# Performance work log

Measured on AMD Instinct MI355X. Metric: run time of the kernel, lower is better.

## Reference

```python
import jax, jax.numpy as jnp
from jax import lax
import numpy as np

# Config mirroring init_kwargs
B, N, PD = 4, 16384, 3
PROJ = 64                 # projection_channel
M1, K1, C1 = 2048, 32, 128  # level-1 SA: fps points, neighbors, out channel
M2, K2, C2 = 512, 32, 256   # level-2 SA
DH, DO = 512, 256           # dense hidden / out (dense_channels)


def fps(pts, M):
    """Farthest point sampling. pts: [N,3] -> indices [M] (starts at point 0)."""
    n = pts.shape[0]
    def step(carry, _):
        dmin, last = carry
        d = jnp.sum((pts - pts[last]) ** 2, axis=-1)   # dist to newest center
        dmin = jnp.minimum(dmin, d)
        nxt = jnp.argmax(dmin).astype(jnp.int32)
        return (dmin, nxt), last
    init = (jnp.full((n,), 1e10, pts.dtype), jnp.int32(0))
    _, idxs = lax.scan(step, init, None, length=M)
    return idxs


def sa_level(pts, feats, M, K, Wa, ba, Wb, bb):
    """PointNet++ set abstraction: FPS + kNN (xyz space) + grouped MLP + max."""
    idx = jax.vmap(lambda p: fps(p, M))(pts)                       # [B,M]
    centers = jnp.take_along_axis(pts, idx[:, :, None], axis=1)    # [B,M,3]
    d = jnp.sum((centers[:, :, None, :] - pts[:, None, :, :]) ** 2, -1)  # [B,M,N]
    _, nidx = lax.top_k(-d, K)                                      # [B,M,K]
    gather = jax.vmap(lambda a, i: a[i])
    rel = gather(pts, nidx) - centers[:, :, None, :]                # [B,M,K,3]
    nf = gather(feats, nidx)                                        # [B,M,K,C]
    g = jnp.concatenate([rel, nf], axis=-1)                         # use_xyz=True
    h = jax.nn.relu(g @ Wa + ba)
    h = jax.nn.relu(h @ Wb + bb)
    return centers, jnp.max(h, axis=2)                              # [B,M,Cout]


def setup_inputs() -> dict:
    key = jax.random.key(0)
    ks = jax.random.split(key, 12)
    w = lambda k, shape, s: jax.random.normal(k, shape, jnp.float32) * s
    z = lambda c: jnp.zeros((c,), jnp.float32)
    return {
        "xyz": jax.random.normal(ks[0], (B, N, PD), jnp.float32),
        "Wp": w(ks[1], (PD, PROJ), 0.3), "bp": z(PROJ),
        "W1a": w(ks[2], (PROJ + 3, C1), 0.1), "b1a": z(C1),
        "W1b": w(ks[3], (C1, C1), 0.08), "b1b": z(C1),
        "W2a": w(ks[4], (C1 + 3, C2), 0.08), "b2a": z(C2),
        "W2b": w(ks[5], (C2, C2), 0.06), "b2b": z(C2),
        "Wd1": w(ks[6], (2 * C2, DH), 0.05), "bd1": z(DH),
        "Wd2": w(ks[7], (DH, DO), 0.05), "bd2": z(DO),
    }


def reference(xyz, Wp, bp, W1a, b1a, W1b, b1b, W2a, b2a, W2b, b2b,
              Wd1, bd1, Wd2, bd2):
    feats = xyz @ Wp + bp            # point_proj: [B,N,PROJ]
    pts = xyz[..., :3]
    pts, feats = sa_level(pts, feats, M1, K1, W1a, b1a, W1b, b1b)
    pts, feats = sa_level(pts, feats, M2, K2, W2a, b2a, W2b, b2b)
    # global max + avg pool (adaptive_max/avg_pool1d to 1), concat -> [B,2*C2]
    g = jnp.concatenate([jnp.max(feats, axis=1), jnp.mean(feats, axis=1)], -1)
    h = jax.nn.relu(g @ Wd1 + bd1)   # DenseBlock w/ activation
    return h @ Wd2 + bd2             # last block: no activation (last_activation=False)
```

## Files before the change

### kernel.cpp

```cpp
#include <hip/hip_runtime.h>

#define B_    4
#define N1_   16384
#define M1_   2048
#define M2_   512
#define KNN_  32
#define PROJ_ 64
#define C1_   128
#define C2_   256
#define PROJ_BLKS_ ((B_ * N1_ * PROJ_) / 512)
#define TAIL_BLKS_ (32 * 512)

__device__ __forceinline__ float sqdist_exact(float px, float py, float pz,
                                              float cx, float cy, float cz) {
    float dx = __fsub_rn(px, cx);
    float dy = __fsub_rn(py, cy);
    float dz = __fsub_rn(pz, cz);
    return __fadd_rn(__fadd_rn(__fmul_rn(dx, dx), __fmul_rn(dy, dy)), __fmul_rn(dz, dz));
}

__device__ __forceinline__ float aload(const float* p) {
    return __uint_as_float(__hip_atomic_load((const unsigned*)p,
                           __ATOMIC_RELAXED, __HIP_MEMORY_SCOPE_AGENT));
}
__device__ __forceinline__ unsigned auload(const unsigned* p) {
    return __hip_atomic_load(p, __ATOMIC_RELAXED, __HIP_MEMORY_SCOPE_AGENT);
}
__device__ __forceinline__ void afence() {
    __builtin_amdgcn_fence(__ATOMIC_ACQUIRE, "agent");
}

#define F_PROG1(f,b)  ((f) + (b) * 16)
#define F_PROG2(f,b)  ((f) + 64 + (b) * 16)
#define F_PROJD(f)    ((f) + 128)
#define F_K1D(f,b,c)  ((f) + 192 + ((b) * 32 + (c)) * 16)
#define F_M2D(f,b)    ((f) + 2240 + (b) * 16)
#define F_K2D(f,b,c)  ((f) + 2304 + ((b) * 8 + (c)) * 16)

__global__ void __launch_bounds__(1024)
sortx_kernel(const float* __restrict__ xyz, float* __restrict__ sx,
             float* __restrict__ sy, float* __restrict__ sz,
             float* __restrict__ sp) {
    const int b = blockIdx.x, t = threadIdx.x;
    const int lane = t & 63, w = t >> 6;
    const float* P = xyz + (size_t)b * N1_ * 3;
    __shared__ int hist[1024];
    __shared__ int wsum[16];
    hist[t] = 0;
    __syncthreads();
    for (int j = t; j < N1_; j += 1024) {
        unsigned kb = __float_as_uint(P[j * 3]);
        kb ^= (kb >> 31) ? 0xFFFFFFFFu : 0x80000000u;
        atomicAdd(&hist[kb >> 22], 1);
    }
    __syncthreads();
    int v = hist[t];
    int cum = v;
    for (int off = 1; off < 64; off <<= 1) {
        int o = __shfl_up(cum, off);
        if (lane >= off) cum += o;
    }
    if (lane == 63) wsum[w] = cum;
    __syncthreads();
    int wpre = 0;
    for (int i = 0; i < w; ++i) wpre += wsum[i];
    const int excl = cum - v + wpre;
    __syncthreads();
    hist[t] = excl;
    __syncthreads();
    for (int j = t; j < N1_; j += 1024) {
        float x = P[j * 3], y = P[j * 3 + 1], z = P[j * 3 + 2];
        unsigned kb = __float_as_uint(x);
        kb ^= (kb >> 31) ? 0xFFFFFFFFu : 0x80000000u;
        int pos = atomicAdd(&hist[kb >> 22], 1);
        size_t o = (size_t)b * N1_ + pos;
        sx[o] = x; sy[o] = y; sz[o] = z;
        float* pr = sp + ((size_t)b * N1_ + pos) * 3;
        pr[0] = x; pr[1] = y; pr[2] = z;
    }
}

typedef float v2f __attribute__((ext_vector_type(2)));

template<int CTRL, int RM>
__device__ __forceinline__ unsigned long long dpp_umax64(unsigned long long pk) {
    unsigned lo = (unsigned)__builtin_amdgcn_update_dpp(
        0, (int)(unsigned)pk, CTRL, RM, 0xf, true);
    unsigned hi = (unsigned)__builtin_amdgcn_update_dpp(
        0, (int)(unsigned)(pk >> 32), CTRL, RM, 0xf, true);
    unsigned long long o = ((unsigned long long)hi << 32) | (unsigned long long)lo;
    return (o > pk) ? o : pk;
}

__device__ __forceinline__ unsigned long long wave_max_key(unsigned long long pk) {
    pk = dpp_umax64<0x111, 0xf>(pk);
    pk = dpp_umax64<0x112, 0xf>(pk);
    pk = dpp_umax64<0x114, 0xf>(pk);
    pk = dpp_umax64<0x118, 0xf>(pk);
    pk = dpp_umax64<0x142, 0xa>(pk);
    pk = dpp_umax64<0x143, 0xc>(pk);
    return pk;
}

__device__ __forceinline__ unsigned reduce8_widx(const unsigned long long* wk,
                                                 int lane) {
    unsigned long long k8 = wk[lane & 7];
    k8 = dpp_umax64<0x111, 0xf>(k8);
    k8 = dpp_umax64<0x112, 0xf>(k8);
    k8 = dpp_umax64<0x114, 0xf>(k8);
    unsigned lo = (unsigned)__builtin_amdgcn_readlane((int)(unsigned)k8, 7);
    return ~lo;
}

__device__ __forceinline__ unsigned reduce4_widx(const unsigned long long* wk,
                                                 int lane) {
    unsigned long long k4 = wk[lane & 3];
    k4 = dpp_umax64<0x111, 0xf>(k4);
    k4 = dpp_umax64<0x112, 0xf>(k4);
    unsigned lo = (unsigned)__builtin_amdgcn_readlane((int)(unsigned)k4, 3);
    return ~lo;
}

template<int N, int NT>
__device__ void knn_bodyT(const float* __restrict__ P,
                          float cx, float cy, float cz,
                          int* __restrict__ out, char* arena) {
    constexpr int K = KNN_;
    constexpr int CAP = 224;
    const int t = threadIdx.x;
    const int lane = t & 63;
    const int w = t >> 6;

    int*      hist = (int*)arena;
    unsigned* eqk  = (unsigned*)(arena + 8192);
    int*      eqi  = (int*)(arena + 8192 + 896);
    int*      wsum = (int*)(arena + 8192 + 1792);
    int*      ctrl = (int*)(arena + 8192 + 1824);

    unsigned prefix = 0; int pbits = 0;
    unsigned Tlo = 0; unsigned long long Thi = 0x100000000ull;
    int L = 0, target = K, Cbin = N;

    for (int round = 0; round < 3; ++round) {
        const int bits  = (round < 2) ? 11 : 10;
        const int nbins = 1 << bits;
        const int shift = 32 - pbits - bits;
        for (int i = t; i < nbins; i += NT) hist[i] = 0;
        __syncthreads();
        for (int j = t; j < N; j += NT) {
            float d = sqdist_exact(P[j * 3], P[j * 3 + 1], P[j * 3 + 2], cx, cy, cz);
            unsigned key = __float_as_uint(d);
            if (key >= Tlo && (unsigned long long)key < Thi)
                atomicAdd(&hist[(key >> shift) & (nbins - 1)], 1);
        }
        __syncthreads();
        const int per = nbins / NT;
        int s = 0;
        for (int i = 0; i < per; ++i) s += hist[t * per + i];
        int cum = s;
        for (int off = 1; off < 64; off <<= 1) {
            int o = __shfl_up(cum, off);
            if (lane >= off) cum += o;
        }
        if (lane == 63) wsum[w] = cum;
        __syncthreads();
        int wpre = 0;
        for (int i = 0; i < w; ++i) wpre += wsum[i];
        cum += wpre;
        const int cumex = cum - s;
        if ((cumex < target) && (cum >= target)) {
            int acc = cumex;
            for (int i = 0; i < per; ++i) {
// ... 108 lines not shown
        const float w2 = Wa[(4 * s4 + 5) * CO + o];
        const float w3 = Wa[(4 * s4 + 6) * CO + o];
#pragma unroll
        for (int k = 0; k < 8; ++k) {
            float4 gv = *(const float4*)&g[k0 + k][4 * s4];
            acc[k] = __fmaf_rn(gv.x, w0, acc[k]);
            acc[k] = __fmaf_rn(gv.y, w1, acc[k]);
            acc[k] = __fmaf_rn(gv.z, w2, acc[k]);
            acc[k] = __fmaf_rn(gv.w, w3, acc[k]);
        }
    }
    {
        const float w0 = Wa[0 * CO + o];
        const float w1 = Wa[1 * CO + o];
        const float w2 = Wa[2 * CO + o];
#pragma unroll
        for (int k = 0; k < 8; ++k) {
            float4 gv = *(const float4*)&g[k0 + k][FD];
            acc[k] = __fmaf_rn(gv.x, w0, acc[k]);
            acc[k] = __fmaf_rn(gv.y, w1, acc[k]);
            acc[k] = __fmaf_rn(gv.z, w2, acc[k]);
        }
    }
#pragma unroll
    for (int k = 0; k < 8; ++k) h1[k0 + k][o] = fmaxf(acc[k], 0.f);
    __syncthreads();
#pragma unroll
    for (int k = 0; k < 8; ++k) acc[k] = bb[o];
    for (int s4 = 0; s4 < CO / 4; ++s4) {
        const float w0 = Wb[(4 * s4 + 0) * CO + o];
        const float w1 = Wb[(4 * s4 + 1) * CO + o];
        const float w2 = Wb[(4 * s4 + 2) * CO + o];
        const float w3 = Wb[(4 * s4 + 3) * CO + o];
#pragma unroll
        for (int k = 0; k < 8; ++k) {
            float4 hv = *(const float4*)&h1[k0 + k][4 * s4];
            acc[k] = __fmaf_rn(hv.x, w0, acc[k]);
            acc[k] = __fmaf_rn(hv.y, w1, acc[k]);
            acc[k] = __fmaf_rn(hv.z, w2, acc[k]);
            acc[k] = __fmaf_rn(hv.w, w3, acc[k]);
        }
    }
    float mx = 0.f;
#pragma unroll
    for (int k = 0; k < 8; ++k) mx = fmaxf(mx, fmaxf(acc[k], 0.f));
    pm[grp][o] = mx;
    __syncthreads();
    if (t < CO) {
        float m0 = fmaxf(fmaxf(pm[0][o], pm[1][o]), fmaxf(pm[2][o], pm[3][o]));
        feats1[bm * CO + o] = m0;
    }
}

__global__ __attribute__((amdgpu_flat_work_group_size(512, 512)))
__attribute__((amdgpu_waves_per_eu(2, 2)))
void mega1_kernel(const float* __restrict__ xyz,
                  const float* __restrict__ sx, const float* __restrict__ sy,
                  const float* __restrict__ sz, const float* __restrict__ sp,
                  const float* __restrict__ Wp, const float* __restrict__ bp,
                  const float* __restrict__ W1a, const float* __restrict__ b1a,
                  const float* __restrict__ W1b, const float* __restrict__ b1b,
                  float* __restrict__ feats0, float* __restrict__ centers1,
                  int* __restrict__ nidx1, float* __restrict__ feats1,
                  unsigned* __restrict__ flags) {
#pragma clang fp contract(off)
    __shared__ alignas(16) char arena[27136];
    asm volatile("" ::: "v255");
    const int bid = blockIdx.x;
    const int t = threadIdx.x;

    if (bid >= B_ + PROJ_BLKS_) {
        const int k = bid - (B_ + PROJ_BLKS_);
        const int c = k >> 9;
        const int r = k & 511;
        const int i = r & 255;
        const int b = (i >> 6) & 3;
        const int m = c * 64 + (i & 63);
        if (r < 256) {
            if (t == 0) {
                while (auload(F_PROG1(flags, b)) <= (unsigned)c)
                    __builtin_amdgcn_s_sleep(16);
            }
            __syncthreads();
            const float* cw = centers1 + ((size_t)b * M1_ + m) * 3;
            float cx = aload(cw + 0), cy = aload(cw + 1), cz = aload(cw + 2);
            knn_bodyT<N1_, 512>(xyz + (size_t)b * N1_ * 3, cx, cy, cz,
                                nidx1 + ((size_t)b * M1_ + m) * KNN_, arena);
            __syncthreads();
            if (t == 0)
                __hip_atomic_fetch_add(F_K1D(flags, b, c), 1u,
                                       __ATOMIC_RELEASE, __HIP_MEMORY_SCOPE_AGENT);
            return;
        }
        if (t == 0) {
            while (auload(F_K1D(flags, b, c)) < 64u ||
                   auload(F_PROJD(flags)) < (unsigned)PROJ_BLKS_)
                __builtin_amdgcn_s_sleep(16);
        }
        __syncthreads();
        afence();
        mlp1_512(b, m, arena, xyz, feats0, centers1, nidx1,
                 W1a, b1a, W1b, b1b, feats1);
        return;
    }
    if (bid >= B_) {
        int tid = (bid - B_) * 512 + t;
        int cc = tid & (PROJ_ - 1);
        int pn = tid >> 6;
        const float* p = xyz + (size_t)pn * 3;
        float acc = p[0] * Wp[0 * PROJ_ + cc];
        acc = __fmaf_rn(p[1], Wp[1 * PROJ_ + cc], acc);
        acc = __fmaf_rn(p[2], Wp[2 * PROJ_ + cc], acc);
        feats0[tid] = acc + bp[cc];
        __syncthreads();
        if (t == 0)
            __hip_atomic_fetch_add(F_PROJD(flags), 1u,
                                   __ATOMIC_RELEASE, __HIP_MEMORY_SCOPE_AGENT);
        return;
    }
    constexpr int NT = 512;
    constexpr int NW = NT / 64;
    constexpr int PPT = N1_ / NT;
    const int b = bid;
    const int w = t >> 6;
    const int lane = t & 63;
    const float* P  = xyz + (size_t)b * N1_ * 3;
    const float* SX = sx + (size_t)b * N1_;
    const float* SY = sy + (size_t)b * N1_;
    const float* SZ = sz + (size_t)b * N1_;
    const float* SP = sp + (size_t)b * N1_ * 3;
    float* C1 = centers1 + (size_t)b * M1_ * 3;
    const int base = t * PPT;
    const unsigned nbase = ~(unsigned)base;

    unsigned long long (*wkey)[NW] = (unsigned long long(*)[NW])arena;
    float* cb1 = (float*)(arena + 128);

    float px[PPT], py[PPT], pz[PPT], dmin[PPT];
#pragma unroll
    for (int k = 0; k < PPT; ++k) {
        px[k] = SX[base + k];
        py[k] = SY[base + k];
        pz[k] = SZ[base + k];
        dmin[k] = 1e10f;
    }
#pragma unroll
    for (int k = 0; k < PPT; ++k)
        asm volatile("" : "+v"(px[k]), "+v"(py[k]), "+v"(pz[k]), "+v"(dmin[k]));

    float xlo = px[0], xhi = px[0];
#pragma unroll
    for (int k = 1; k < PPT; ++k) {
        xlo = fminf(xlo, px[k]);
        xhi = fmaxf(xhi, px[k]);
    }
    for (int off = 1; off < 64; off <<= 1) {
        xlo = fminf(xlo, __shfl_xor(xlo, off));
        xhi = fmaxf(xhi, __shfl_xor(xhi, off));
    }

    unsigned long long mykey = ((unsigned long long)__float_as_uint(1e10f) << 32);
    float cx = P[0], cy = P[1], cz = P[2];

    for (int m = 0; m < M1_; ++m) {
        if (t == 0) {
            cb1[m * 3 + 0] = cx; cb1[m * 3 + 1] = cy; cb1[m * 3 + 2] = cz;
        }
        if ((m & 63) == 63) {
            __syncthreads();
            const int c = m >> 6;
            if (t < 48)
                ((float4*)C1)[c * 48 + t] = ((const float4*)cb1)[c * 48 + t];
            __syncthreads();
            if (t == 0)
                __hip_atomic_store(F_PROG1(flags, b), (unsigned)(c + 1),
                                   __ATOMIC_RELEASE, __HIP_MEMORY_SCOPE_AGENT);
        }
        if (m == M1_ - 1) break;
        const int par = m & 1;
        const float UBval = __uint_as_float((unsigned)(mykey >> 32));
        const float dxs = fmaxf(fmaxf(xlo - cx, cx - xhi), 0.0f);
        if (!(0.999f * (dxs * dxs) >= UBval)) {
            unsigned long long pk = 0;
#pragma unroll
            for (int k = 0; k < PPT; ++k) {
                float d  = sqdist_exact(px[k], py[k], pz[k], cx, cy, cz);
                float nd = fminf(dmin[k], d);
                dmin[k] = nd;
                unsigned long long kk =
                    ((unsigned long long)__float_as_uint(nd) << 32) |
                    (unsigned)(nbase - (unsigned)k);
                pk = (kk > pk) ? kk : pk;
            }
            pk = wave_max_key(pk);
            unsigned klo = (unsigned)__builtin_amdgcn_readlane((int)(unsigned)pk, 63);
            unsigned khi = (unsigned)__builtin_amdgcn_readlane((int)(unsigned)(pk >> 32), 63);
            mykey = ((unsigned long long)khi << 32) | klo;
        }
        if (lane == 63) wkey[par][w] = mykey;
        __syncthreads();
        const unsigned widx = reduce8_widx(wkey[par], lane);
        const float* cp = SP + (size_t)widx * 3;
        cx = cp[0]; cy = cp[1]; cz = cp[2];
    }
}

__device__ __forceinline__ void fps2_body(const float* __restrict__ centers1,
                                          float* __restrict__ centers2,
                                          unsigned* __restrict__ flags,
                                          char* arena) {
#pragma clang fp contract(off)
    constexpr int NT = 256;
    constexpr int NW = 4;
    constexpr int NP = (M1_ / NT) / 2;
    const int b = blockIdx.x;
    const int t = threadIdx.x;
    const int w = t >> 6;
    const int lane = t & 63;
    const float* P = centers1 + (size_t)b * M1_ * 3;
    float* C = centers2 + (size_t)b * M2_ * 3;

    unsigned long long (*wkey)[NW] = (unsigned long long(*)[NW])arena;
    float* cb2 = (float*)(arena + 64);

    v2f px2[NP], py2[NP], pz2[NP];
    float dmin[2 * NP];
#pragma unroll
    for (int p = 0; p < NP; ++p) {
        const int j0 = (2 * p) * NT + t;
        const int j1 = j0 + NT;
        px2[p] = (v2f){P[j0 * 3 + 0], P[j1 * 3 + 0]};
        py2[p] = (v2f){P[j0 * 3 + 1], P[j1 * 3 + 1]};
        pz2[p] = (v2f){P[j0 * 3 + 2], P[j1 * 3 + 2]};
        dmin[2 * p] = 1e10f; dmin[2 * p + 1] = 1e10f;
    }
#pragma unroll
    for (int p = 0; p < NP; ++p)
        asm volatile("" : "+v"(px2[p]), "+v"(py2[p]), "+v"(pz2[p]));

    float cx = P[0], cy = P[1], cz = P[2];

    for (int m = 0; m < M2_; ++m) {
        if (t == 0) {
            cb2[m * 3 + 0] = cx; cb2[m * 3 + 1] = cy; cb2[m * 3 + 2] = cz;
        }
        if ((m & 63) == 63) {
            __syncthreads();
            const int c = m >> 6;
            if (t < 48)
                ((float4*)C)[c * 48 + t] = ((const float4*)cb2)[c * 48 + t];
            __syncthreads();
            if (t == 0)
                __hip_atomic_store(F_PROG2(flags, b), (unsigned)(c + 1),
                                   __ATOMIC_RELEASE, __HIP_MEMORY_SCOPE_AGENT);
        }
        if (m == M2_ - 1) break;
        const int par = m & 1;
        const v2f c2x = {cx, cx}, c2y = {cy, cy}, c2z = {cz, cz};
        float bv = -1.0f; int bk = 0;
#pragma unroll
        for (int p = 0; p < NP; ++p) {
            v2f dx = px2[p] - c2x;
            v2f dy = py2[p] - c2y;
            v2f dz = pz2[p] - c2z;
            v2f d2 = (dx * dx + dy * dy) + dz * dz;
            float nd0 = fminf(dmin[2 * p],     d2.x);
            float nd1 = fminf(dmin[2 * p + 1], d2.y);
            dmin[2 * p]     = nd0;
            dmin[2 * p + 1] = nd1;
            bool g0 = nd0 > bv; bv = g0 ? nd0 : bv; bk = g0 ? 2 * p     : bk;
            bool g1 = nd1 > bv; bv = g1 ? nd1 : bv; bk = g1 ? 2 * p + 1 : bk;
        }
        unsigned gi = (unsigned)(bk * NT + t);
        unsigned long long pk =
            ((unsigned long long)__float_as_uint(bv) << 32) | (unsigned)(~gi);
        pk = wave_max_key(pk);
        if (lane == 63) wkey[par][w] = pk;
        __syncthreads();
        const unsigned widx = reduce4_widx(wkey[par], lane);
        const float* cp = P + (size_t)widx * 3;
        cx = cp[0]; cy = cp[1]; cz = cp[2];
    }
}

template<int NPTS, int FD, int CO, int M>
__device__ __forceinline__ void mlp_body(int bm, char* arena,
                 const float* __restrict__ pts, const float* __restrict__ feats,
                 const float* __restrict__ centers, const int* __restrict__ nidx,
                 const float* __restrict__ Wa, const float* __restrict__ ba,
                 const float* __restrict__ Wb, const float* __restrict__ bb,
                 float* __restrict__ outf) {
    constexpr int KN = KNN_;
    constexpr int GS = FD + 4;
    const int b = bm / M;
    const int t = threadIdx.x;
    float (*g)[GS]  = (float(*)[GS])arena;
    float (*h1)[CO] = (float(*)[CO])(arena + sizeof(float) * KN * GS);
    const int* nb = nidx + (size_t)bm * KN;
    const float* cen = centers + (size_t)bm * 3;
    const float cx = cen[0], cy = cen[1], cz = cen[2];
    {
        constexpr int PARTS = CO / KN;
        constexpr int CHUNK = FD / PARTS;
        const int kk = t / PARTS;
        const int q  = t % PARTS;
        const int j  = nb[kk];
        const float* f = feats + ((size_t)b * NPTS + j) * FD + q * CHUNK;
        float* gr = &g[kk][q * CHUNK];
#pragma unroll
        for (int u = 0; u < CHUNK / 4; ++u)
            *(float4*)(gr + 4 * u) = *(const float4*)(f + 4 * u);
        if (q == 0) {
            const float* p = pts + ((size_t)b * NPTS + j) * 3;
            g[kk][FD + 0] = __fsub_rn(p[0], cx);
            g[kk][FD + 1] = __fsub_rn(p[1], cy);
            g[kk][FD + 2] = __fsub_rn(p[2], cz);
            g[kk][FD + 3] = 0.f;
        }
    }
    __syncthreads();
    const int o = t;
    float acc[KN];
#pragma unroll
    for (int k = 0; k < KN; ++k) acc[k] = ba[o];
    for (int s4 = 0; s4 < FD / 4; ++s4) {
        const float w0 = Wa[(4 * s4 + 3) * CO + o];
        const float w1 = Wa[(4 * s4 + 4) * CO + o];
        const float w2 = Wa[(4 * s4 + 5) * CO + o];
        const float w3 = Wa[(4 * s4 + 6) * CO + o];
#pragma unroll
        for (int k = 0; k < KN; ++k) {
            float4 gv = *(const float4*)&g[k][4 * s4];
            acc[k] = __fmaf_rn(gv.x, w0, acc[k]);
            acc[k] = __fmaf_rn(gv.y, w1, acc[k]);
            acc[k] = __fmaf_rn(gv.z, w2, acc[k]);
            acc[k] = __fmaf_rn(gv.w, w3, acc[k]);
        }
    }
    {
        const float w0 = Wa[0 * CO + o];
        const float w1 = Wa[1 * CO + o];
        const float w2 = Wa[2 * CO + o];
#pragma unroll
        for (int k = 0; k < KN; ++k) {
            float4 gv = *(const float4*)&g[k][FD];
            acc[k] = __fmaf_rn(gv.x, w0, acc[k]);
            acc[k] = __fmaf_rn(gv.y, w1, acc[k]);
            acc[k] = __fmaf_rn(gv.z, w2, acc[k]);
        }
    }
#pragma unroll
    for (int k = 0; k < KN; ++k) h1[k][o] = fmaxf(acc[k], 0.f);
    __syncthreads();
#pragma unroll
    for (int k = 0; k < KN; ++k) acc[k] = bb[o];
    for (int s4 = 0; s4 < CO / 4; ++s4) {
        const float w0 = Wb[(4 * s4 + 0) * CO + o];
        const float w1 = Wb[(4 * s4 + 1) * CO + o];
        const float w2 = Wb[(4 * s4 + 2) * CO + o];
        const float w3 = Wb[(4 * s4 + 3) * CO + o];
#pragma unroll
        for (int k = 0; k < KN; ++k) {
            float4 hv = *(const float4*)&h1[k][4 * s4];
            acc[k] = __fmaf_rn(hv.x, w0, acc[k]);
            acc[k] = __fmaf_rn(hv.y, w1, acc[k]);
            acc[k] = __fmaf_rn(hv.z, w2, acc[k]);
            acc[k] = __fmaf_rn(hv.w, w3, acc[k]);
        }
    }
    float mx = 0.f;
#pragma unroll
    for (int k = 0; k < KN; ++k) mx = fmaxf(mx, fmaxf(acc[k], 0.f));
    outf[(size_t)bm * CO + o] = mx;
}

__global__ void __launch_bounds__(C2_)
sa2_kernel(const float* __restrict__ centers1, const float* __restrict__ feats1,
           float* __restrict__ centers2, int* __restrict__ nidx2,
           const float* __restrict__ W2a, const float* __restrict__ b2a,
           const float* __restrict__ W2b, const float* __restrict__ b2b,
           const float* __restrict__ Wd1, const float* __restrict__ bd1,
           const float* __restrict__ Wd2, const float* __restrict__ bd2,
           float* __restrict__ feats2, float* __restrict__ outp,
           unsigned* __restrict__ flags) {
    constexpr size_t BYTES = sizeof(float) * (KNN_ * (C1_ + 4) + KNN_ * C2_);
    __shared__ alignas(16) char arena[BYTES];
    const int bid = blockIdx.x;
    const int t = threadIdx.x;
    if (bid < B_) {
        fps2_body(centers1, centers2, flags, arena);
        return;
    }
    const int kk = bid - B_;
    if (kk < 8 * 512) {
        const int c = kk >> 9;
        const int r = kk & 511;
        const int i = r & 255;
        const int b = (i >> 6) & 3;
        const int m = c * 64 + (i & 63);
        if (r < 256) {
            if (t == 0) {
                while (auload(F_PROG2(flags, b)) <= (unsigned)c)
                    __builtin_amdgcn_s_sleep(16);
            }
            __syncthreads();
            const float* cw = centers2 + ((size_t)b * M2_ + m) * 3;
            float cx = aload(cw + 0), cy = aload(cw + 1), cz = aload(cw + 2);
            knn_bodyT<M1_, 256>(centers1 + (size_t)b * M1_ * 3, cx, cy, cz,
                                nidx2 + ((size_t)b * M2_ + m) * KNN_, arena);
            __syncthreads();
            if (t == 0)
                __hip_atomic_fetch_add(F_K2D(flags, b, c), 1u,
                                       __ATOMIC_RELEASE, __HIP_MEMORY_SCOPE_AGENT);
            return;
        }
        if (t == 0) {
            while (auload(F_K2D(flags, b, c)) < 64u)
                __builtin_amdgcn_s_sleep(16);
        }
        __syncthreads();
        afence();
        mlp_body<M1_, C1_, C2_, M2_>((int)((size_t)b * M2_ + m), arena,
                                     centers1, feats1, centers2, nidx2,
                                     W2a, b2a, W2b, b2b, feats2);
        __syncthreads();
        if (t == 0)
            __hip_atomic_fetch_add(F_M2D(flags, b), 1u,
                                   __ATOMIC_RELEASE, __HIP_MEMORY_SCOPE_AGENT);
        return;
    }
    const int b = kk - 8 * 512;
    if (t == 0) {
        while (auload(F_M2D(flags, b)) < (unsigned)M2_)
            __builtin_amdgcn_s_sleep(16);
    }
    __syncthreads();
    afence();
    float* gsh = (float*)arena;
    float* hsh = (float*)(arena + 2048);
    const float* F = feats2 + (size_t)b * M2_ * C2_;
    float mx = -1e30f, sm = 0.f;
    for (int r = 0; r < M2_; ++r) {
        float v = F[r * C2_ + t];
        mx = fmaxf(mx, v);
        sm += v;
    }
    gsh[t] = mx;
    gsh[C2_ + t] = sm * (1.0f / (float)M2_);
    __syncthreads();
#pragma unroll
    for (int oo = 0; oo < 2; ++oo) {
        const int o = t + oo * 256;
        float acc = bd1[o];
        for (int i = 0; i < 512; ++i)
            acc = __fmaf_rn(gsh[i], Wd1[i * 512 + o], acc);
        hsh[o] = fmaxf(acc, 0.f);
    }
    __syncthreads();
    float acc = bd2[t];
    for (int i = 0; i < 512; ++i)
        acc = __fmaf_rn(hsh[i], Wd2[i * 256 + t], acc);
    outp[b * 256 + t] = acc;
}

extern "C" void kernel_launch(void* const* d_in, const int* in_sizes, int n_in,
                              void* d_out, int out_size, void* d_ws, size_t ws_size,
                              hipStream_t stream) {
    const float* xyz = (const float*)d_in[0];
    const float* Wp  = (const float*)d_in[1];
    const float* bp  = (const float*)d_in[2];
    const float* W1a = (const float*)d_in[3];
    const float* b1a = (const float*)d_in[4];
    const float* W1b = (const float*)d_in[5];
    const float* b1b = (const float*)d_in[6];
    const float* W2a = (const float*)d_in[7];
    const float* b2a = (const float*)d_in[8];
    const float* W2b = (const float*)d_in[9];
    const float* b2b = (const float*)d_in[10];
    const float* Wd1 = (const float*)d_in[11];
    const float* bd1 = (const float*)d_in[12];
    const float* Wd2 = (const float*)d_in[13];
    const float* bd2 = (const float*)d_in[14];
    float* out = (float*)d_out;

    char* ws = (char*)d_ws;
    size_t off = 0;
    auto alloc = [&](size_t bytes) { void* p = ws + off; off += (bytes + 255) & ~(size_t)255; return p; };
    float* feats0   = (float*)alloc((size_t)B_ * N1_ * PROJ_ * 4);
    float* centers1 = (float*)alloc((size_t)B_ * M1_ * 3 * 4);
    int*   nidx1    = (int*)  alloc((size_t)B_ * M1_ * KNN_ * 4);
    float* feats1   = (float*)alloc((size_t)B_ * M1_ * C1_ * 4);
    float* centers2 = (float*)alloc((size_t)B_ * M2_ * 3 * 4);
    int*   nidx2    = (int*)  alloc((size_t)B_ * M2_ * KNN_ * 4);
    float* feats2   = (float*)alloc((size_t)B_ * M2_ * C2_ * 4);
    unsigned* flags = (unsigned*)alloc(16384);
    float* sx       = (float*)alloc((size_t)B_ * N1_ * 4);
    float* sy       = (float*)alloc((size_t)B_ * N1_ * 4);
    float* sz       = (float*)alloc((size_t)B_ * N1_ * 4);
    float* sp       = (float*)alloc((size_t)B_ * N1_ * 3 * 4);
    (void)in_sizes; (void)n_in; (void)out_size; (void)ws_size;

    hipMemsetAsync(flags, 0, 16384, stream);

    sortx_kernel<<<dim3(B_), dim3(1024), 0, stream>>>(xyz, sx, sy, sz, sp);
    mega1_kernel<<<dim3(B_ + PROJ_BLKS_ + TAIL_BLKS_), dim3(512), 0, stream>>>(
        xyz, sx, sy, sz, sp, Wp, bp, W1a, b1a, W1b, b1b,
        feats0, centers1, nidx1, feats1, flags);
    sa2_kernel<<<dim3(B_ + 8 * 512 + B_), dim3(C2_), 0, stream>>>(
        centers1, feats1, centers2, nidx2, W2a, b2a, W2b, b2b,
        Wd1, bd1, Wd2, bd2, feats2, out, flags);
}
```

Baseline: 3.152 ms.

## Fuse level-2 set abstraction and dense head into single persistent mega kernel

Merges the second kernel (level-2 FPS, kNN, MLP, pooling and dense head) into the level-1 mega kernel. The FPS block now runs level-2 FPS right after level-1 using centers kept in shared memory, and new block ranges handle kNN2, MLP2 and the head, coordinated through flag counters including a new per-batch MLP1-done flag. This removes the kernel boundary and lets level-2 work overlap the tail of level 1. The cost is a larger shared arena, which may reduce occupancy, and more spin-waiting dependencies that rely on dispatch ordering to avoid deadlock.

Result: slower. 3.252 ms (+3.2%).

```diff
diff --git a/kernel.cpp b/kernel.cpp
--- a/kernel.cpp
+++ b/kernel.cpp
@@ -8,8 +8,11 @@
 #define PROJ_ 64
 #define C1_   128
 #define C2_   256
-#define PROJ_BLKS_ ((B_ * N1_ * PROJ_) / 512)
-#define TAIL_BLKS_ (32 * 512)
+#define PROJ_OFF_  4
+#define TAIL1_OFF_ (PROJ_OFF_ + 8192)
+#define TAIL2_OFF_ (TAIL1_OFF_ + 32 * 512)
+#define HEAD_OFF_  (TAIL2_OFF_ + 8 * 512)
+#define TOTAL_BLKS_ (HEAD_OFF_ + B_)
 
 __device__ __forceinline__ float sqdist_exact(float px, float py, float pz,
                                               float cx, float cy, float cz) {
@@ -36,6 +39,7 @@
 #define F_K1D(f,b,c)  ((f) + 192 + ((b) * 32 + (c)) * 16)
 #define F_M2D(f,b)    ((f) + 2240 + (b) * 16)
 #define F_K2D(f,b,c)  ((f) + 2304 + ((b) * 8 + (c)) * 16)
+#define F_M1D(f,b)    ((f) + 2816 + (b) * 16)
 
 __global__ void __launch_bounds__(1024)
 sortx_kernel(const float* __restrict__ xyz, float* __restrict__ sx,
@@ -109,15 +113,6 @@
     k8 = dpp_umax64<0x112, 0xf>(k8);
     k8 = dpp_umax64<0x114, 0xf>(k8);
     unsigned lo = (unsigned)__builtin_amdgcn_readlane((int)(unsigned)k8, 7);
-    return ~lo;
-}
-
-__device__ __forceinline__ unsigned reduce4_widx(const unsigned long long* wk,
-                                                 int lane) {
-    unsigned long long k4 = wk[lane & 3];
-    k4 = dpp_umax64<0x111, 0xf>(k4);
-    k4 = dpp_umax64<0x112, 0xf>(k4);
-    unsigned lo = (unsigned)__builtin_amdgcn_readlane((int)(unsigned)k4, 3);
     return ~lo;
 }
 
@@ -332,25 +327,205 @@
     }
 }
 
+__device__ void mlp2_512(int b, int m, char* arena,
+                         const float* __restrict__ centers1,
+                         const float* __restrict__ feats1,
+                         const float* __restrict__ centers2,
+                         const int* __restrict__ nidx2,
+                         const float* __restrict__ Wa, const float* __restrict__ ba,
+                         const float* __restrict__ Wb, const float* __restrict__ bb,
+                         float* __restrict__ feats2) {
+    constexpr int KN = KNN_, FD = C1_, CO = C2_, GS = FD + 4;
+    const int t = threadIdx.x;
+    const size_t bm = (size_t)b * M2_ + m;
+    float (*g)[GS]  = (float(*)[GS])arena;
+    float (*h1)[CO] = (float(*)[CO])(arena + 16896);
+    float (*pm)[CO] = (float(*)[CO])(arena + 16896 + 32768);
+    const int* nb = nidx2 + bm * KN;
+    const float* cen = centers2 + bm * 3;
+    const float cx = cen[0], cy = cen[1], cz = cen[2];
+    {
+        const int kk = t >> 4;
+        const int q  = t & 15;
+        const int j  = nb[kk];
+        const float* f = feats1 + ((size_t)b * M1_ + j) * FD + q * 8;
+        *(float4*)&g[kk][q * 8]     = *(const float4*)f;
+        *(float4*)&g[kk][q * 8 + 4] = *(const float4*)(f + 4);
+        if (q == 0) {
+            const float* p = centers1 + ((size_t)b * M1_ + j) * 3;
+            g[kk][FD + 0] = __fsub_rn(p[0], cx);
+            g[kk][FD + 1] = __fsub_rn(p[1], cy);
+            g[kk][FD + 2] = __fsub_rn(p[2], cz);
+            g[kk][FD + 3] = 0.f;
+        }
+    }
+    __syncthreads();
+    const int o = t & (CO - 1);
+    const int grp = t >> 8;
+    const int k0 = grp * 16;
+    float acc[16];
+#pragma unroll
+    for (int k = 0; k < 16; ++k) acc[k] = ba[o];
+    for (int s4 = 0; s4 < FD / 4; ++s4) {
+        const float w0 = Wa[(4 * s4 + 3) * CO + o];
+        const float w1 = Wa[(4 * s4 + 4) * CO + o];
+        const float w2 = Wa[(4 * s4 + 5) * CO + o];
+        const float w3 = Wa[(4 * s4 + 6) * CO + o];
+#pragma unroll
+        for (int k = 0; k < 16; ++k) {
+            float4 gv = *(const float4*)&g[k0 + k][4 * s4];
+            acc[k] = __fmaf_rn(gv.x, w0, acc[k]);
+            acc[k] = __fmaf_rn(gv.y, w1, acc[k]);
+            acc[k] = __fmaf_rn(gv.z, w2, acc[k]);
+            acc[k] = __fmaf_rn(gv.w, w3, acc[k]);
+        }
+    }
+    {
+        const float w0 = Wa[0 * CO + o];
+        const float w1 = Wa[1 * CO + o];
+        const float w2 = Wa[2 * CO + o];
+#pragma unroll
+        for (int k = 0; k < 16; ++k) {
+            float4 gv = *(const float4*)&g[k0 + k][FD];
+            acc[k] = __fmaf_rn(gv.x, w0, acc[k]);
+            acc[k] = __fmaf_rn(gv.y, w1, acc[k]);
+            acc[k] = __fmaf_rn(gv.z, w2, acc[k]);
+        }
+    }
+#pragma unroll
+    for (int k = 0; k < 16; ++k) h1[k0 + k][o] = fmaxf(acc[k], 0.f);
+    __syncthreads();
+#pragma unroll
+    for (int k = 0; k < 16; ++k) acc[k] = bb[o];
+    for (int s4 = 0; s4 < CO / 4; ++s4) {
+        const float w0 = Wb[(4 * s4 + 0) * CO + o];
+        const float w1 = Wb[(4 * s4 + 1) * CO + o];
+        const float w2 = Wb[(4 * s4 + 2) * CO + o];
+        const float w3 = Wb[(4 * s4 + 3) * CO + o];
+#pragma unroll
+        for (int k = 0; k < 16; ++k) {
+            float4 hv = *(const float4*)&h1[k0 + k][4 * s4];
+            acc[k] = __fmaf_rn(hv.x, w0, acc[k]);
+            acc[k] = __fmaf_rn(hv.y, w1, acc[k]);
+            acc[k] = __fmaf_rn(hv.z, w2, acc[k]);
+            acc[k] = __fmaf_rn(hv.w, w3, acc[k]);
+        }
+    }
+    float mx = 0.f;
+#pragma unroll
+    for (int k = 0; k < 16; ++k) mx = fmaxf(mx, fmaxf(acc[k], 0.f));
+    pm[grp][o] = mx;
+    __syncthreads();
+    if (t < CO) {
+        feats2[bm * CO + o] = fmaxf(pm[0][o], pm[1][o]);
+    }
+}
+
 __global__ __attribute__((amdgpu_flat_work_group_size(512, 512)))
 __attribute__((amdgpu_waves_per_eu(2, 2)))
-void mega1_kernel(const float* __restrict__ xyz,
-                  const float* __restrict__ sx, const float* __restrict__ sy,
-                  const float* __restrict__ sz, const float* __restrict__ sp,
-                  const float* __restrict__ Wp, const float* __restrict__ bp,
-                  const float* __restrict__ W1a, const float* __restrict__ b1a,
-                  const float* __restrict__ W1b, const float* __restrict__ b1b,
-                  float* __restrict__ feats0, float* __restrict__ centers1,
-                  int* __restrict__ nidx1, float* __restrict__ feats1,
-                  unsigned* __restrict__ flags) {
+void mega_kernel(const float* __restrict__ xyz,
+                 const float* __restrict__ sx, const float* __restrict__ sy,
+                 const float* __restrict__ sz, const float* __restrict__ sp,
+                 const float* __restrict__ Wp, const float* __restrict__ bp,
+                 const float* __restrict__ W1a, const float* __restrict__ b1a,
+                 const float* __restrict__ W1b, const float* __restrict__ b1b,
+                 const float* __restrict__ W2a, const float* __restrict__ b2a,
+                 const float* __restrict__ W2b, const float* __restrict__ b2b,
+                 const float* __restrict__ Wd1, const float* __restrict__ bd1,
+                 const float* __restrict__ Wd2, const float* __restrict__ bd2,
+                 float* __restrict__ feats0, float* __restrict__ centers1,
+                 int* __restrict__ nidx1, float* __restrict__ feats1,
+                 float* __restrict__ centers2, int* __restrict__ nidx2,
+                 float* __restrict__ feats2, float* __restrict__ outp,
+                 unsigned* __restrict__ flags) {
 #pragma clang fp contract(off)
-    __shared__ alignas(16) char arena[27136];
+    __shared__ alignas(16) char arena[51712];
     asm volatile("" ::: "v255");
     const int bid = blockIdx.x;
     const int t = threadIdx.x;
 
-    if (bid >= B_ + PROJ_BLKS_) {
-        const int k = bid - (B_ + PROJ_BLKS_);
+    if (bid >= HEAD_OFF_) {
+        const int b = bid - HEAD_OFF_;
+        if (t == 0) {
+            while (auload(F_M2D(flags, b)) < (unsigned)M2_)
+                __builtin_amdgcn_s_sleep(16);
+        }
+        __syncthreads();
+        afence();
+        float* gsh = (float*)arena;
+        float* hsh = (float*)(arena + 2048);
+        const float* F = feats2 + (size_t)b * M2_ * C2_;
+        if (t < C2_) {
+            float mx = -1e30f, sm = 0.f;
+            for (int r = 0; r < M2_; ++r) {
+                float v = F[r * C2_ + t];
+                mx = fmaxf(mx, v);
+                sm += v;
+            }
+            gsh[t] = mx;
+            gsh[C2_ + t] = sm * (1.0f / (float)M2_);
+        }
+        __syncthreads();
+        if (t < C2_) {
+#pragma unroll
+            for (int oo = 0; oo < 2; ++oo) {
+                const int o = t + oo * 256;
+                float acc = bd1[o];
+                for (int i = 0; i < 512; ++i)
+                    acc = __fmaf_rn(gsh[i], Wd1[i * 512 + o], acc);
+                hsh[o] = fmaxf(acc, 0.f);
+            }
+        }
+        __syncthreads();
+        if (t < C2_) {
+            float acc = bd2[t];
+            for (int i = 0; i < 512; ++i)
+                acc = __fmaf_rn(hsh[i], Wd2[i * 256 + t], acc);
+            outp[b * 256 + t] = acc;
+        }
+        return;
+    }
+    if (bid >= TAIL2_OFF_) {
+        const int k = bid - TAIL2_OFF_;
+        const int c = k >> 9;
+        const int r = k & 511;
+        const int i = r & 255;
+        const int b = (i >> 6) & 3;
+        const int m = c * 64 + (i & 63);
+        if (r < 256) {
+            if (t == 0) {
+                while (auload(F_PROG2(flags, b)) <= (unsigned)c)
+                    __builtin_amdgcn_s_sleep(16);
+            }
+            __syncthreads();
+            afence();
+            const float* cw = centers2 + ((size_t)b * M2_ + m) * 3;
+            float cx = cw[0], cy = cw[1], cz = cw[2];
+            knn_bodyT<M1_, 512>(centers1 + (size_t)b * M1_ * 3, cx, cy, cz,
+                                nidx2 + ((size_t)b * M2_ + m) * KNN_, arena);
+            __syncthreads();
+            if (t == 0)
+                __hip_atomic_fetch_add(F_K2D(flags, b, c), 1u,
+                                       __ATOMIC_RELEASE, __HIP_MEMORY_SCOPE_AGENT);
+            return;
+        }
+        if (t == 0) {
+            while (auload(F_K2D(flags, b, c)) < 64u ||
+                   auload(F_M1D(flags, b)) < (unsigned)M1_)
+                __builtin_amdgcn_s_sleep(16);
+        }
+        __syncthreads();
+        afence();
+        mlp2_512(b, m, arena, centers1, feats1, centers2, nidx2,
+                 W2a, b2a, W2b, b2b, feats2);
+        __syncthreads();
+        if (t == 0)
+            __hip_atomic_fetch_add(F_M2D(flags, b), 1u,
+                                   __ATOMIC_RELEASE, __HIP_MEMORY_SCOPE_AGENT);
+        return;
+    }
+    if (bid >= TAIL1_OFF_) {
+        const int k = bid - TAIL1_OFF_;
         const int c = k >> 9;
         const int r = k & 511;
         const int i = r & 255;
@@ -374,13 +549,17 @@
         }
         if (t == 0) {
             while (auload(F_K1D(flags, b, c)) < 64u ||
-                   auload(F_PROJD(flags)) < (unsigned)PROJ_BLKS_)
+                   auload(F_PROJD(flags)) < 8192u)
                 __builtin_amdgcn_s_sleep(16);
         }
         __syncthreads();
         afence();
         mlp1_512(b, m, arena, xyz, feats0, centers1, nidx1,
                  W1a, b1a, W1b, b1b, feats1);
+        __syncthreads();
+        if (t == 0)
+            __hip_atomic_fetch_add(F_M1D(flags, b), 1u,
+                                   __ATOMIC_RELEASE, __HIP_MEMORY_SCOPE_AGENT);
         return;
     }
     if (bid >= B_) {
@@ -400,7 +579,6 @@
     }
     constexpr int NT = 512;
     constexpr int NW = NT / 64;
-    constexpr int PPT = N1_ / NT;
     const int b = bid;
     const int w = t >> 6;
     const int lane = t & 63;
@@ -410,337 +588,148 @@
     const float* SZ = sz + (size_t)b * N1_;
     const float* SP = sp + (size_t)b * N1_ * 3;
     float* C1 = centers1 + (size_t)b * M1_ * 3;
-    const int base = t * PPT;
-    const unsigned nbase = ~(unsigned)base;
+    float* C2 = centers2 + (size_t)b * M2_ * 3;
 
     unsigned long long (*wkey)[NW] = (unsigned long long(*)[NW])arena;
     float* cb1 = (float*)(arena + 128);
-
-    float px[PPT], py[PPT], pz[PPT], dmin[PPT];
-#pragma unroll
-    for (int k = 0; k < PPT; ++k) {
-        px[k] = SX[base + k];
-        py[k] = SY[base + k];
-        pz[k] = SZ[base + k];
-        dmin[k] = 1e10f;
-    }
-#pragma unroll
-    for (int k = 0; k < PPT; ++k)
-        asm volatile("" : "+v"(px[k]), "+v"(py[k]), "+v"(pz[k]), "+v"(dmin[k]));
-
-    float xlo = px[0], xhi = px[0];
-#pragma unroll
-    for (int k = 1; k < PPT; ++k) {
-        xlo = fminf(xlo, px[k]);
-        xhi = fmaxf(xhi, px[k]);
-    }
-    for (int off = 1; off < 64; off <<= 1) {
-        xlo = fminf(xlo, __shfl_xor(xlo, off));
-        xhi = fmaxf(xhi, __shfl_xor(xhi, off));
-    }
-
-    unsigned long long mykey = ((unsigned long long)__float_as_uint(1e10f) << 32);
-    float cx = P[0], cy = P[1], cz = P[2];
-
-    for (int m = 0; m < M1_; ++m) {
-        if (t == 0) {
-            cb1[m * 3 + 0] = cx; cb1[m * 3 + 1] = cy; cb1[m * 3 + 2] = cz;
-        }
-        if ((m & 63) == 63) {
+    float* cb2 = (float*)(arena + 24704);
+
+    {
+        constexpr int PPT = N1_ / NT;
+        const int base = t * PPT;
+        const unsigned nbase = ~(unsigned)base;
+
+        float px[PPT], py[PPT], pz[PPT], dmin[PPT];
+#pragma unroll
+        for (int k = 0; k < PPT; ++k) {
+            px[k] = SX[base + k];
+            py[k] = SY[base + k];
+            pz[k] = SZ[base + k];
+            dmin[k] = 1e10f;
+        }
+#pragma unroll
+        for (int k = 0; k < PPT; ++k)
+            asm volatile("" : "+v"(px[k]), "+v"(py[k]), "+v"(pz[k]), "+v"(dmin[k]));
+
+        float xlo = px[0], xhi = px[0];
+#pragma unroll
+        for (int k = 1; k < PPT; ++k) {
+            xlo = fminf(xlo, px[k]);
+            xhi = fmaxf(xhi, px[k]);
+        }
+        for (int off = 1; off < 64; off <<= 1) {
+            xlo = fminf(xlo, __shfl_xor(xlo, off));
+            xhi = fmaxf(xhi, __shfl_xor(xhi, off));
+        }
+
+        unsigned long long mykey = ((unsigned long long)__float_as_uint(1e10f) << 32);
+        float cx = P[0], cy = P[1], cz = P[2];
+
+        for (int m = 0; m < M1_; ++m) {
+            if (t == 0) {
+                cb1[m * 3 + 0] = cx; cb1[m * 3 + 1] = cy; cb1[m * 3 + 2] = cz;
+            }
+            if ((m & 63) == 63) {
+                __syncthreads();
+                const int c = m >> 6;
+                if (t < 48)
+                    ((float4*)C1)[c * 48 + t] = ((const float4*)cb1)[c * 48 + t];
+                __syncthreads();
+                if (t == 0)
+                    __hip_atomic_store(F_PROG1(flags, b), (unsigned)(c + 1),
+                                       __ATOMIC_RELEASE, __HIP_MEMORY_SCOPE_AGENT);
+            }
+            if (m == M1_ - 1) break;
+            const int par = m & 1;
+            const float UBval = __uint_as_float((unsigned)(mykey >> 32));
+            const float dxs = fmaxf(fmaxf(xlo - cx, cx - xhi), 0.0f);
+            if (!(0.999f * (dxs * dxs) >= UBval)) {
+                unsigned long long pk = 0;
+#pragma unroll
+                for (int k = 0; k < PPT; ++k) {
+                    float d  = sqdist_exact(px[k], py[k], pz[k], cx, cy, cz);
+                    float nd = fminf(dmin[k], d);
+                    dmin[k] = nd;
+                    unsigned long long kk =
+                        ((unsigned long long)__float_as_uint(nd) << 32) |
+                        (unsigned)(nbase - (unsigned)k);
+                    pk = (kk > pk) ? kk : pk;
+                }
+                pk = wave_max_key(pk);
+                unsigned klo = (unsigned)__builtin_amdgcn_readlane((int)(unsigned)pk, 63);
+                unsigned khi = (unsigned)__builtin_amdgcn_readlane((int)(unsigned)(pk >> 32), 63);
+                mykey = ((unsigned long long)khi << 32) | klo;
+            }
+            if (lane == 63) wkey[par][w] = mykey;
             __syncthreads();
-            const int c = m >> 6;
-            if (t < 48)
-                ((float4*)C1)[c * 48 + t] = ((const float4*)cb1)[c * 48 + t];
+            const unsigned widx = reduce8_widx(wkey[par], lane);
+            const float* cp = SP + (size_t)widx * 3;
+            cx = cp[0]; cy = cp[1]; cz = cp[2];
+        }
+    }
+    __syncthreads();
+    {
+        constexpr int NP = (M1_ / NT) / 2;
+        v2f px2[NP], py2[NP], pz2[NP];
+        float dmin[2 * NP];
+#pragma unroll
+        for (int p = 0; p < NP; ++p) {
+            const int j0 = (2 * p) * NT + t;
+            const int j1 = j0 + NT;
+            px2[p] = (v2f){cb1[j0 * 3 + 0], cb1[j1 * 3 + 0]};
+            py2[p] = (v2f){cb1[j0 * 3 + 1], cb1[j1 * 3 + 1]};
+            pz2[p] = (v2f){cb1[j0 * 3 + 2], cb1[j1 * 3 + 2]};
+            dmin[2 * p] = 1e10f; dmin[2 * p + 1] = 1e10f;
+        }
+#pragma unroll
+        for (int p = 0; p < NP; ++p)
+            asm volatile("" : "+v"(px2[p]), "+v"(py2[p]), "+v"(pz2[p]));
+
+        float cx = cb1[0], cy = cb1[1], cz = cb1[2];
+
+        for (int m = 0; m < M2_; ++m) {
+            if (t == 0) {
+                cb2[m * 3 + 0] = cx; cb2[m * 3 + 1] = cy; cb2[m * 3 + 2] = cz;
+            }
+            if ((m & 63) == 63) {
+                __syncthreads();
+                const int c = m >> 6;
+                if (t < 48)
+                    ((float4*)C2)[c * 48 + t] = ((const float4*)cb2)[c * 48 + t];
+                __syncthreads();
+                if (t == 0)
+                    __hip_atomic_store(F_PROG2(flags, b), (unsigned)(c + 1),
+                                       __ATOMIC_RELEASE, __HIP_MEMORY_SCOPE_AGENT);
+            }
+            if (m == M2_ - 1) break;
+            const int par = m & 1;
+            const v2f c2x = {cx, cx}, c2y = {cy, cy}, c2z = {cz, cz};
+            float bv = -1.0f; int bk = 0;
+#pragma unroll
+            for (int p = 0; p < NP; ++p) {
+                v2f dx = px2[p] - c2x;
+                v2f dy = py2[p] - c2y;
+                v2f dz = pz2[p] - c2z;
+                v2f d2 = (dx * dx + dy * dy) + dz * dz;
+                float nd0 = fminf(dmin[2 * p],     d2.x);
+                float nd1 = fminf(dmin[2 * p + 1], d2.y);
+                dmin[2 * p]     = nd0;
+                dmin[2 * p + 1] = nd1;
+                bool g0 = nd0 > bv; bv = g0 ? nd0 : bv; bk = g0 ? 2 * p     : bk;
+                bool g1 = nd1 > bv; bv = g1 ? nd1 : bv; bk = g1 ? 2 * p + 1 : bk;
+            }
+            unsigned gi = (unsigned)(bk * NT + t);
+            unsigned long long pk =
+                ((unsigned long long)__float_as_uint(bv) << 32) | (unsigned)(~gi);
+            pk = wave_max_key(pk);
+            if (lane == 63) wkey[par][w] = pk;
             __syncthreads();
-            if (t == 0)
-                __hip_atomic_store(F_PROG1(flags, b), (unsigned)(c + 1),
-                                   __ATOMIC_RELEASE, __HIP_MEMORY_SCOPE_AGENT);
-        }
-        if (m == M1_ - 1) break;
-        const int par = m & 1;
-        const float UBval = __uint_as_float((unsigned)(mykey >> 32));
-        const float dxs = fmaxf(fmaxf(xlo - cx, cx - xhi), 0.0f);
-        if (!(0.999f * (dxs * dxs) >= UBval)) {
-            unsigned long long pk = 0;
-#pragma unroll
-            for (int k = 0; k < PPT; ++k) {
-                float d  = sqdist_exact(px[k], py[k], pz[k], cx, cy, cz);
-                float nd = fminf(dmin[k], d);
-                dmin[k] = nd;
-                unsigned long long kk =
-                    ((unsigned long long)__float_as_uint(nd) << 32) |
-                    (unsigned)(nbase - (unsigned)k);
-                pk = (kk > pk) ? kk : pk;
-            }
-            pk = wave_max_key(pk);
-            unsigned klo = (unsigned)__builtin_amdgcn_readlane((int)(unsigned)pk, 63);
-            unsigned khi = (unsigned)__builtin_amdgcn_readlane((int)(unsigned)(pk >> 32), 63);
-            mykey = ((unsigned long long)khi << 32) | klo;
-        }
-        if (lane == 63) wkey[par][w] = mykey;
-        __syncthreads();
-        const unsigned widx = reduce8_widx(wkey[par], lane);
-        const float* cp = SP + (size_t)widx * 3;
-        cx = cp[0]; cy = cp[1]; cz = cp[2];
-    }
-}
-
-__device__ __forceinline__ void fps2_body(const float* __restrict__ centers1,
-                                          float* __restrict__ centers2,
-                                          unsigned* __restrict__ flags,
-                                          char* arena) {
-#pragma clang fp contract(off)
-    constexpr int NT = 256;
-    constexpr int NW = 4;
-    constexpr int NP = (M1_ / NT) / 2;
-    const int b = blockIdx.x;
-    const int t = threadIdx.x;
-    const int w = t >> 6;
-    const int lane = t & 63;
-    const float* P = centers1 + (size_t)b * M1_ * 3;
-    float* C = centers2 + (size_t)b * M2_ * 3;
-
-    unsigned long long (*wkey)[NW] = (unsigned long long(*)[NW])arena;
-    float* cb2 = (float*)(arena + 64);
-
-    v2f px2[NP], py2[NP], pz2[NP];
-    float dmin[2 * NP];
-#pragma unroll
-    for (int p = 0; p < NP; ++p) {
-        const int j0 = (2 * p) * NT + t;
-        const int j1 = j0 + NT;
-        px2[p] = (v2f){P[j0 * 3 + 0], P[j1 * 3 + 0]};
-        py2[p] = (v2f){P[j0 * 3 + 1], P[j1 * 3 + 1]};
-        pz2[p] = (v2f){P[j0 * 3 + 2], P[j1 * 3 + 2]};
-        dmin[2 * p] = 1e10f; dmin[2 * p + 1] = 1e10f;
-    }
-#pragma unroll
-    for (int p = 0; p < NP; ++p)
-        asm volatile("" : "+v"(px2[p]), "+v"(py2[p]), "+v"(pz2[p]));
-
-    float cx = P[0], cy = P[1], cz = P[2];
-
-    for (int m = 0; m < M2_; ++m) {
-        if (t == 0) {
-            cb2[m * 3 + 0] = cx; cb2[m * 3 + 1] = cy; cb2[m * 3 + 2] = cz;
-        }
-        if ((m & 63) == 63) {
-            __syncthreads();
-            const int c = m >> 6;
-            if (t < 48)
-                ((float4*)C)[c * 48 + t] = ((const float4*)cb2)[c * 48 + t];
-            __syncthreads();
-            if (t == 0)
-                __hip_atomic_store(F_PROG2(flags, b), (unsigned)(c + 1),
-                                   __ATOMIC_RELEASE, __HIP_MEMORY_SCOPE_AGENT);
-        }
-        if (m == M2_ - 1) break;
-        const int par = m & 1;
-        const v2f c2x = {cx, cx}, c2y = {cy, cy}, c2z = {cz, cz};
-        float bv = -1.0f; int bk = 0;
-#pragma unroll
-        for (int p = 0; p < NP; ++p) {
-            v2f dx = px2[p] - c2x;
-            v2f dy = py2[p] - c2y;
-            v2f dz = pz2[p] - c2z;
-            v2f d2 = (dx * dx + dy * dy) + dz * dz;
-            float nd0 = fminf(dmin[2 * p],     d2.x);
-            float nd1 = fminf(dmin[2 * p + 1], d2.y);
-            dmin[2 * p]     = nd0;
-            dmin[2 * p + 1] = nd1;
-            bool g0 = nd0 > bv; bv = g0 ? nd0 : bv; bk = g0 ? 2 * p     : bk;
-            bool g1 = nd1 > bv; bv = g1 ? nd1 : bv; bk = g1 ? 2 * p + 1 : bk;
-        }
-        unsigned gi = (unsigned)(bk * NT + t);
-        unsigned long long pk =
-            ((unsigned long long)__float_as_uint(bv) << 32) | (unsigned)(~gi);
-        pk = wave_max_key(pk);
-        if (lane == 63) wkey[par][w] = pk;
-        __syncthreads();
-        const unsigned widx = reduce4_widx(wkey[par], lane);
-        const float* cp = P + (size_t)widx * 3;
-        cx = cp[0]; cy = cp[1]; cz = cp[2];
-    }
-}
-
-template<int NPTS, int FD, int CO, int M>
-__device__ __forceinline__ void mlp_body(int bm, char* arena,
-                 const float* __restrict__ pts, const float* __restrict__ feats,
-                 const float* __restrict__ centers, const int* __restrict__ nidx,
-                 const float* __restrict__ Wa, const float* __restrict__ ba,
-                 const float* __restrict__ Wb, const float* __restrict__ bb,
-                 float* __restrict__ outf) {
-    constexpr int KN = KNN_;
-    constexpr int GS = FD + 4;
-    const int b = bm / M;
-    const int t = threadIdx.x;
-    float (*g)[GS]  = (float(*)[GS])arena;
-    float (*h1)[CO] = (float(*)[CO])(arena + sizeof(float) * KN * GS);
-    const int* nb = nidx + (size_t)bm * KN;
-    const float* cen = centers + (size_t)bm * 3;
-    const float cx = cen[0], cy = cen[1], cz = cen[2];
-    {
-        constexpr int PARTS = CO / KN;
-        constexpr int CHUNK = FD / PARTS;
-        const int kk = t / PARTS;
-        const int q  = t % PARTS;
-        const int j  = nb[kk];
-        const float* f = feats + ((size_t)b * NPTS + j) * FD + q * CHUNK;
-        float* gr = &g[kk][q * CHUNK];
-#pragma unroll
-        for (int u = 0; u < CHUNK / 4; ++u)
-            *(float4*)(gr + 4 * u) = *(const float4*)(f + 4 * u);
-        if (q == 0) {
-            const float* p = pts + ((size_t)b * NPTS + j) * 3;
-            g[kk][FD + 0] = __fsub_rn(p[0], cx);
-            g[kk][FD + 1] = __fsub_rn(p[1], cy);
-            g[kk][FD + 2] = __fsub_rn(p[2], cz);
-            g[kk][FD + 3] = 0.f;
-        }
-    }
-    __syncthreads();
-    const int o = t;
-    float acc[KN];
-#pragma unroll
-    for (int k = 0; k < KN; ++k) acc[k] = ba[o];
-    for (int s4 = 0; s4 < FD / 4; ++s4) {
-        const float w0 = Wa[(4 * s4 + 3) * CO + o];
-        const float w1 = Wa[(4 * s4 + 4) * CO + o];
-        const float w2 = Wa[(4 * s4 + 5) * CO + o];
-        const float w3 = Wa[(4 * s4 + 6) * CO + o];
-#pragma unroll
-        for (int k = 0; k < KN; ++k) {
-            float4 gv = *(const float4*)&g[k][4 * s4];
-            acc[k] = __fmaf_rn(gv.x, w0, acc[k]);
-            acc[k] = __fmaf_rn(gv.y, w1, acc[k]);
-            acc[k] = __fmaf_rn(gv.z, w2, acc[k]);
-            acc[k] = __fmaf_rn(gv.w, w3, acc[k]);
-        }
-    }
-    {
-        const float w0 = Wa[0 * CO + o];
-        const float w1 = Wa[1 * CO + o];
-        const float w2 = Wa[2 * CO + o];
-#pragma unroll
-        for (int k = 0; k < KN; ++k) {
-            float4 gv = *(const float4*)&g[k][FD];
-            acc[k] = __fmaf_rn(gv.x, w0, acc[k]);
-            acc[k] = __fmaf_rn(gv.y, w1, acc[k]);
-            acc[k] = __fmaf_rn(gv.z, w2, acc[k]);
-        }
-    }
-#pragma unroll
-    for (int k = 0; k < KN; ++k) h1[k][o] = fmaxf(acc[k], 0.f);
-    __syncthreads();
-#pragma unroll
-    for (int k = 0; k < KN; ++k) acc[k] = bb[o];
-    for (int s4 = 0; s4 < CO / 4; ++s4) {
-        const float w0 = Wb[(4 * s4 + 0) * CO + o];
-        const float w1 = Wb[(4 * s4 + 1) * CO + o];
-        const float w2 = Wb[(4 * s4 + 2) * CO + o];
-        const float w3 = Wb[(4 * s4 + 3) * CO + o];
-#pragma unroll
-        for (int k = 0; k < KN; ++k) {
-            float4 hv = *(const float4*)&h1[k][4 * s4];
-            acc[k] = __fmaf_rn(hv.x, w0, acc[k]);
-            acc[k] = __fmaf_rn(hv.y, w1, acc[k]);
-            acc[k] = __fmaf_rn(hv.z, w2, acc[k]);
-            acc[k] = __fmaf_rn(hv.w, w3, acc[k]);
-        }
-    }
-    float mx = 0.f;
-#pragma unroll
-    for (int k = 0; k < KN; ++k) mx = fmaxf(mx, fmaxf(acc[k], 0.f));
-    outf[(size_t)bm * CO + o] = mx;
-}
-
-__global__ void __launch_bounds__(C2_)
-sa2_kernel(const float* __restrict__ centers1, const float* __restrict__ feats1,
-           float* __restrict__ centers2, int* __restrict__ nidx2,
-           const float* __restrict__ W2a, const float* __restrict__ b2a,
-           const float* __restrict__ W2b, const float* __restrict__ b2b,
-           const float* __restrict__ Wd1, const float* __restrict__ bd1,
-           const float* __restrict__ Wd2, const float* __restrict__ bd2,
-           float* __restrict__ feats2, float* __restrict__ outp,
-           unsigned* __restrict__ flags) {
-    constexpr size_t BYTES = sizeof(float) * (KNN_ * (C1_ + 4) + KNN_ * C2_);
-    __shared__ alignas(16) char arena[BYTES];
-    const int bid = blockIdx.x;
-    const int t = threadIdx.x;
-    if (bid < B_) {
-        fps2_body(centers1, centers2, flags, arena);
-        return;
-    }
-    const int kk = bid - B_;
-    if (kk < 8 * 512) {
-        const int c = kk >> 9;
-        const int r = kk & 511;
-        const int i = r & 255;
-        const int b = (i >> 6) & 3;
-        const int m = c * 64 + (i & 63);
-        if (r < 256) {
-            if (t == 0) {
-                while (auload(F_PROG2(flags, b)) <= (unsigned)c)
-                    __builtin_amdgcn_s_sleep(16);
-            }
-            __syncthreads();
-            const float* cw = centers2 + ((size_t)b * M2_ + m) * 3;
-            float cx = aload(cw + 0), cy = aload(cw + 1), cz = aload(cw + 2);
-            knn_bodyT<M1_, 256>(centers1 + (size_t)b * M1_ * 3, cx, cy, cz,
-                                nidx2 + ((size_t)b * M2_ + m) * KNN_, arena);
-            __syncthreads();
-            if (t == 0)
-                __hip_atomic_fetch_add(F_K2D(flags, b, c), 1u,
-                                       __ATOMIC_RELEASE, __HIP_MEMORY_SCOPE_AGENT);
-            return;
-        }
-        if (t == 0) {
-            while (auload(F_K2D(flags, b, c)) < 64u)
-                __builtin_amdgcn_s_sleep(16);
-        }
-        __syncthreads();
-        afence();
-        mlp_body<M1_, C1_, C2_, M2_>((int)((size_t)b * M2_ + m), arena,
-                                     centers1, feats1, centers2, nidx2,
-                                     W2a, b2a, W2b, b2b, feats2);
-        __syncthreads();
-        if (t == 0)
-            __hip_atomic_fetch_add(F_M2D(flags, b), 1u,
-                                   __ATOMIC_RELEASE, __HIP_MEMORY_SCOPE_AGENT);
-        return;
-    }
-    const int b = kk - 8 * 512;
-    if (t == 0) {
-        while (auload(F_M2D(flags, b)) < (unsigned)M2_)
-            __builtin_amdgcn_s_sleep(16);
-    }
-    __syncthreads();
-    afence();
-    float* gsh = (float*)arena;
-    float* hsh = (float*)(arena + 2048);
-    const float* F = feats2 + (size_t)b * M2_ * C2_;
-    float mx = -1e30f, sm = 0.f;
-    for (int r = 0; r < M2_; ++r) {
-        float v = F[r * C2_ + t];
-        mx = fmaxf(mx, v);
-        sm += v;
-    }
-    gsh[t] = mx;
-    gsh[C2_ + t] = sm * (1.0f / (float)M2_);
-    __syncthreads();
-#pragma unroll
-    for (int oo = 0; oo < 2; ++oo) {
-        const int o = t + oo * 256;
-        float acc = bd1[o];
-        for (int i = 0; i < 512; ++i)
-            acc = __fmaf_rn(gsh[i], Wd1[i * 512 + o], acc);
-        hsh[o] = fmaxf(acc, 0.f);
-    }
-    __syncthreads();
-    float acc = bd2[t];
-    for (int i = 0; i < 512; ++i)
-        acc = __fmaf_rn(hsh[i], Wd2[i * 256 + t], acc);
-    outp[b * 256 + t] = acc;
+            const unsigned widx = reduce8_widx(wkey[par], lane);
+            cx = cb1[widx * 3 + 0];
+            cy = cb1[widx * 3 + 1];
+            cz = cb1[widx * 3 + 2];
+        }
+    }
 }
 
 extern "C" void kernel_launch(void* const* d_in, const int* in_sizes, int n_in,
@@ -783,10 +772,8 @@
     hipMemsetAsync(flags, 0, 16384, stream);
 
     sortx_kernel<<<dim3(B_), dim3(1024), 0, stream>>>(xyz, sx, sy, sz, sp);
-    mega1_kernel<<<dim3(B_ + PROJ_BLKS_ + TAIL_BLKS_), dim3(512), 0, stream>>>(
+    mega_kernel<<<dim3(TOTAL_BLKS_), dim3(512), 0, stream>>>(
         xyz, sx, sy, sz, sp, Wp, bp, W1a, b1a, W1b, b1b,
-        feats0, centers1, nidx1, feats1, flags);
-    sa2_kernel<<<dim3(B_ + 8 * 512 + B_), dim3(C2_), 0, stream>>>(
-        centers1, feats1, centers2, nidx2, W2a, b2a, W2b, b2b,
-        Wd1, bd1, Wd2, bd2, feats2, out, flags);
-}
+        W2a, b2a, W2b, b2b, Wd1, bd1, Wd2, bd2,
+        feats0, centers1, nidx1, feats1, centers2, nidx2, feats2, out, flags);
+}
```
